# Kernel optimization log

Measured on AMD Instinct MI355X. Metric: run time of the kernel, lower is better.

## Reference

```python
import jax, jax.numpy as jnp
import numpy as np

B, NP1, D = 64, 1025, 256  # N+1 tokens, feature dim d (label dim makes d+1)
N_LAYER, N_HEAD = 4, 4
VAR = 0.02


def _pad_pq(allparam):
    """Build padded (d+1)x(d+1) P_full/Q_full for all layers/heads at once.
    P_full gets a 1 at [d, d]; Q_full is zero-padded."""
    L, H, _, d, _ = allparam.shape
    Pf = (jnp.zeros((L, H, d + 1, d + 1), allparam.dtype)
          .at[:, :, :d, :d].set(allparam[:, :, 0])
          .at[:, :, d, d].set(1.0))
    Qf = (jnp.zeros((L, H, d + 1, d + 1), allparam.dtype)
          .at[:, :, :d, :d].set(allparam[:, :, 1]))
    return Pf, Qf


def setup_inputs() -> dict:
    key = jax.random.key(0)
    k1, k2 = jax.random.split(key)
    Z = jax.random.normal(k1, (B, NP1, D + 1), dtype=jnp.float32)
    allparam = jax.random.normal(k2, (N_LAYER, N_HEAD, 2, D, D), dtype=jnp.float32) * VAR
    return {"Z": Z, "allparam": allparam}


def reference(Z, allparam):
    Bb, Np1, dp1 = Z.shape
    N = Np1 - 1
    Pf, Qf = _pad_pq(allparam)  # (L, H, d+1, d+1)
    # mask A = diag(1,...,1,0): equivalent to zeroing the last key token
    mask = jnp.ones((Np1,), Z.dtype).at[N].set(0.0)
    for l in range(allparam.shape[0]):
        # attn[b,h,n,m] = Z[b,n,:] @ Q_full[h] @ Z[b,m,:]
        attn = jnp.einsum('bni,hij,bmj->bhnm', Z, Qf[l], Z)
        attn = jax.nn.relu(attn)
        # key[b,h,m,i] = P_full[h] @ Z[b,m,:], last token masked out (A matrix)
        key_t = jnp.einsum('hij,bmj->bhmi', Pf[l], Z) * mask[None, None, :, None]
        # sum over heads fused into the einsum reduction; scale by 1/N
        res = jnp.einsum('bhnm,bhmi->bni', attn, key_t) / N
        Z = Z + res  # residual connection
    return Z
```

## Files before the change

kernel.cpp:

```cpp
#include <hip/hip_runtime.h>
#include <cstdint>
#include <cstddef>

#define B_    64
#define NP1   1025
#define N_    1024
#define D_    256
#define DP1   257
#define L_    4
#define H_    4
#define MT    1024
#define NCHE  32
#define IPAD  272
#define TR_   1024

typedef __bf16 bf16;
typedef bf16 bf16x4 __attribute__((ext_vector_type(4)));
typedef bf16 bf16x8 __attribute__((ext_vector_type(8)));
typedef float f32x4 __attribute__((ext_vector_type(4)));

__device__ __forceinline__ f32x4 mfma16(bf16x8 a, bf16x8 b, f32x4 c) {
    return __builtin_amdgcn_mfma_f32_16x16x32_bf16(a, b, c, 0, 0, 0);
}

__device__ __forceinline__ void async16(const void* g, void* l) {
    __builtin_amdgcn_global_load_lds(
        (const __attribute__((address_space(1))) void*)g,
        (__attribute__((address_space(3))) void*)l, 16, 0, 0);
}

__global__ void k_prep_pq(const float* __restrict__ ap,
                          bf16* __restrict__ Pb, bf16* __restrict__ Qt) {
    int idx = blockIdx.x * 256 + threadIdx.x;
    int j  = idx & 255;
    int i  = (idx >> 8) & 255;
    int lh = idx >> 16;
    const float* base = ap + (size_t)lh * 2 * D_ * D_;
    float p = base[i * D_ + j];
    float q = base[D_ * D_ + i * D_ + j];
    Pb[((size_t)lh * D_ + i) * D_ + j] = (bf16)p;
    Qt[((size_t)lh * D_ + j) * D_ + i] = (bf16)q;
}

__global__ __launch_bounds__(256) void k_zbt(const float* __restrict__ Z,
                                             bf16* __restrict__ Zb,
                                             bf16* __restrict__ ZbT) {
    __shared__ float t[64][65];
    int m0 = blockIdx.x * 64, j0 = blockIdx.y * 64, b = blockIdx.z;
    int c = threadIdx.x & 63, r0 = threadIdx.x >> 6;
#pragma unroll
    for (int s = 0; s < 16; s++) {
        int r = s * 4 + r0;
        int j = j0 + c;
        float v = (j < DP1) ? Z[((size_t)b * NP1 + m0 + r) * DP1 + j] : 0.f;
        t[r][c] = v;
        if (j < D_) Zb[((size_t)b * N_ + m0 + r) * D_ + j] = (bf16)v;
    }
    __syncthreads();
#pragma unroll
    for (int s = 0; s < 16; s++) {
        int rr = s * 4 + r0;
        int j = j0 + rr;
        if (j < DP1)
            ZbT[((size_t)b * DP1 + j) * MT + m0 + c] = (bf16)t[c][rr];
    }
}

__global__ __launch_bounds__(512, 1) void k_attn(const bf16* __restrict__ Zb,
                                                 const bf16* __restrict__ ZbT,
                                                 const bf16* __restrict__ Qt,
                                                 const bf16* __restrict__ Pb,
                                                 float* __restrict__ Z,
                                                 bf16* __restrict__ T,
                                                 bf16* __restrict__ Tlab,
                                                 int layer) {
    __shared__ bf16 zbS[2][32][256];
    __shared__ bf16 ztS[2][IPAD][32];
    __shared__ bf16 sl[8][32][40];

    const int tid  = threadIdx.x;
    const int id   = blockIdx.x;
    const int wave = tid >> 6, lane = tid & 63;
    const int quad = lane >> 4, l16 = lane & 15;

    const int xcd = id & 7, u = id >> 3;
    const int b   = xcd + 8 * (u & 7);
    const int bx  = u >> 3;
    const int n0w = bx * 256 + wave * 32;

    const bf16* Zbb  = Zb  + (size_t)b * N_ * D_;
    const bf16* ZbTb = ZbT + (size_t)b * DP1 * MT;

    const int zrow  = wave * 2 + (lane >> 5);
    const int zscol = ((lane & 31) ^ (zrow & 7)) * 8;
    const int krow  = wave * 16 + (lane >> 2);
    const int kscol = ((lane & 3) ^ ((lane >> 3) & 3)) * 8;
    const int xs    = l16 & 7;
    const int kf    = (l16 >> 1) & 3;

    auto stage = [&](int mc_, int p_) {
        int m0 = mc_ * 32;
        const bf16* zsrc = Zbb + (size_t)(m0 + zrow) * D_ + zscol;
#pragma unroll
        for (int t = 0; t < 2; t++)
            async16(zsrc + (size_t)t * 16 * D_, &zbS[p_][t * 16 + wave * 2][0]);
        const bf16* ksrc = ZbTb + (size_t)krow * MT + m0 + kscol;
#pragma unroll
        for (int t = 0; t < 2; t++)
            async16(ksrc + (size_t)t * 128 * MT, &ztS[p_][t * 128 + wave * 16][0]);
        if (wave == 0)
            async16(ksrc + (size_t)256 * MT, &ztS[p_][256][0]);
    };

    int p = 0;

    for (int h = 0; h < H_; h++) {
        const bf16* Qth = Qt + (size_t)(layer * H_ + h) * D_ * D_;

        if (h == 0) stage(0, 0);

        f32x4 acc[2][17];
#pragma unroll
        for (int ns = 0; ns < 2; ns++)
#pragma unroll
            for (int it = 0; it < 17; it++) acc[ns][it] = (f32x4){0.f, 0.f, 0.f, 0.f};

        bf16x8 zqa[2][8];
#pragma unroll 2
        for (int jc = 0; jc < 8; jc++) {
            f32x4 c00 = (f32x4){0.f,0.f,0.f,0.f}, c01 = c00, c10 = c00, c11 = c00;
#pragma unroll
            for (int kc = 0; kc < 8; kc++) {
                const bf16* qb = Qth + (size_t)(jc * 32 + l16) * D_ + kc * 32 + quad * 8;
                const bf16* az = Zbb + (size_t)(n0w + l16) * D_ + kc * 32 + quad * 8;
                bf16x8 q0 = *(const bf16x8*)(qb);
                bf16x8 q1 = *(const bf16x8*)(qb + 16 * D_);
                bf16x8 a0 = *(const bf16x8*)(az);
                bf16x8 a1 = *(const bf16x8*)(az + 16 * D_);
                c00 = mfma16(q0, a0, c00);
                c01 = mfma16(q0, a1, c01);
                c10 = mfma16(q1, a0, c10);
                c11 = mfma16(q1, a1, c11);
            }
            f32x4 cv[2][2] = {{c00, c01}, {c10, c11}};
#pragma unroll
            for (int jt = 0; jt < 2; jt++)
#pragma unroll
                for (int ns = 0; ns < 2; ns++) {
                    bf16x4 pk;
#pragma unroll
                    for (int r = 0; r < 4; r++) pk[r] = (bf16)cv[jt][ns][r];
                    *(bf16x4*)(&sl[wave][ns * 16 + l16][jt * 16 + quad * 4]) = pk;
                }
#pragma unroll
            for (int ns = 0; ns < 2; ns++)
                zqa[ns][jc] = *(const bf16x8*)(&sl[wave][ns * 16 + l16][quad * 8]);
        }

        if (h == 0) {
            asm volatile("s_waitcnt vmcnt(0)" ::: "memory");
            __builtin_amdgcn_s_barrier();
            __builtin_amdgcn_sched_barrier(0);
        }

        for (int cc = 0; cc < NCHE; cc++) {
            const bool haveNext = (cc + 1 < NCHE);
            if (haveNext) {
                int mcn = (h & 1) ? (NCHE - 2 - cc) : (cc + 1);
                stage(mcn, p ^ 1);
                if (wave == 0) asm volatile("s_waitcnt vmcnt(5)" ::: "memory");
                else           asm volatile("s_waitcnt vmcnt(4)" ::: "memory");
            } else {
                asm volatile("s_waitcnt vmcnt(0)" ::: "memory");
            }
            __builtin_amdgcn_s_barrier();
            __builtin_amdgcn_sched_barrier(0);

#pragma unroll
            for (int mt = 0; mt < 2; mt++) {
                f32x4 st0 = (f32x4){0.f,0.f,0.f,0.f}, st1 = st0;
                const bf16* zr = &zbS[p][mt * 16 + l16][0];
                __builtin_amdgcn_s_setprio(1);
#pragma unroll
                for (int kc = 0; kc < 8; kc++) {
                    bf16x8 az = *(const bf16x8*)(zr + (((kc * 4 + quad) ^ xs) * 8));
                    st0 = mfma16(az, zqa[0][kc], st0);
                    st1 = mfma16(az, zqa[1][kc], st1);
                }
                __builtin_amdgcn_s_setprio(0);
                bf16x4 p0, p1;
#pragma unroll
                for (int r = 0; r < 4; r++) {
                    p0[r] = (bf16)(st0[r] > 0.f ? st0[r] : 0.f);
                    p1[r] = (bf16)(st1[r] > 0.f ? st1[r] : 0.f);
                }
                *(bf16x4*)(&sl[wave][l16][mt * 16 + quad * 4])      = p0;
                *(bf16x4*)(&sl[wave][16 + l16][mt * 16 + quad * 4]) = p1;
            }
            bf16x8 sfrag[2];
#pragma unroll
            for (int ns = 0; ns < 2; ns++)
                sfrag[ns] = *(const bf16x8*)(&sl[wave][ns * 16 + l16][quad * 8]);

            __builtin_amdgcn_s_setprio(1);
#pragma unroll
            for (int it = 0; it < 17; it++) {
                const bf16* kr = &ztS[p][it * 16 + l16][0];
                bf16x8 bk = *(const bf16x8*)(kr + ((quad ^ kf) * 8));
                acc[0][it] = mfma16(sfrag[0], bk, acc[0][it]);
                acc[1][it] = mfma16(sfrag[1], bk, acc[1][it]);
            }
            __builtin_amdgcn_s_setprio(0);

            __builtin_amdgcn_sched_barrier(0);
            __builtin_amdgcn_s_barrier();
            if (haveNext) p ^= 1;
        }

        bf16* Th  = T    + (size_t)(b * H_ + h) * TR_ * D_;
        bf16* Tlh = Tlab + (size_t)(b * H_ + h) * TR_;
#pragma unroll
        for (int ns = 0; ns < 2; ns++)
#pragma unroll
            for (int it = 0; it < 17; it++)
#pragma unroll
                for (int r = 0; r < 4; r++) {
                    int n = n0w + ns * 16 + quad * 4 + r;
                    float v = acc[ns][it][r];
                    if (it < 16)
                        Th[(size_t)n * D_ + it * 16 + l16] = (bf16)v;
                    else if (l16 == 0)
                        Tlh[n] = (bf16)v;
                }
    }

    __syncthreads();
    {
        f32x4 acc2[2][16];
#pragma unroll
        for (int ns = 0; ns < 2; ns++)
#pragma unroll
            for (int it = 0; it < 16; it++) acc2[ns][it] = (f32x4){0.f, 0.f, 0.f, 0.f};

        for (int h = 0; h < H_; h++) {
            const bf16* Th = T  + (size_t)(b * H_ + h) * TR_ * D_;
            const bf16* Ph = Pb + (size_t)(layer * H_ + h) * D_ * D_;
#pragma unroll 2
            for (int kc = 0; kc < 8; kc++) {
                bf16x8 af[2];
#pragma unroll
                for (int ns = 0; ns < 2; ns++) {
                    int row = n0w + ns * 16 + l16;
                    af[ns] = *(const bf16x8*)(Th + (size_t)row * D_ + kc * 32 + quad * 8);
                }
#pragma unroll
                for (int it = 0; it < 16; it++) {
                    bf16x8 bp = *(const bf16x8*)(Ph + (size_t)(it * 16 + l16) * D_ + kc * 32 + quad * 8);
                    acc2[0][it] = mfma16(af[0], bp, acc2[0][it]);
                    acc2[1][it] = mfma16(af[1], bp, acc2[1][it]);
                }
            }
        }

        const float inv = 1.0f / (float)N_;
#pragma unroll
        for (int ns = 0; ns < 2; ns++)
#pragma unroll
            for (int it = 0; it < 16; it++) {
                const int i = it * 16 + l16;
                const int nbase = n0w + ns * 16 + quad * 4;
#pragma unroll
                for (int r = 0; r < 4; r++) {
                    size_t zi = ((size_t)b * NP1 + nbase + r) * DP1 + i;
                    Z[zi] += acc2[ns][it][r] * inv;
                }
            }
        if (tid < 256) {
            int n = bx * 256 + tid;
            float s = 0.f;
#pragma unroll
            for (int h = 0; h < H_; h++)
                s += (float)Tlab[(size_t)(b * H_ + h) * TR_ + n];
            Z[((size_t)b * NP1 + n) * DP1 + D_] += s * inv;
        }
    }

    if (bx == 0) {
        __syncthreads();
        float* lz1 = (float*)&zbS[0][0][0];
        float* lzq = lz1 + 256;
        float* lsS = lzq + 1024;
        float* lT  = lsS + 4096;
        if (tid < 256) lz1[tid] = Z[((size_t)b * NP1 + N_) * DP1 + tid];
        __syncthreads();
        {
            int j = tid & 255, hh = tid >> 8;
            for (int h2 = hh; h2 < H_; h2 += 2) {
                const bf16* qr = Qt + ((size_t)(layer * H_ + h2) * D_ + j) * D_;
                float a = 0.f;
                for (int i8 = 0; i8 < 32; i8++) {
                    bf16x8 q = *(const bf16x8*)(qr + i8 * 8);
#pragma unroll
                    for (int k = 0; k < 8; k++) a += lz1[i8 * 8 + k] * (float)q[k];
                }
                lzq[h2 * 256 + j] = a;
            }
        }
        __syncthreads();
        for (int m = tid; m < N_; m += 512) {
            const bf16* zr = Zbb + (size_t)m * D_;
            float a0 = 0.f, a1 = 0.f, a2 = 0.f, a3 = 0.f;
            for (int j8 = 0; j8 < 32; j8++) {
                bf16x8 z8 = *(const bf16x8*)(zr + j8 * 8);
#pragma unroll
                for (int k = 0; k < 8; k++) {
                    float zv = (float)z8[k];
                    int j = j8 * 8 + k;
                    a0 += lzq[j] * zv;
                    a1 += lzq[256 + j] * zv;
                    a2 += lzq[512 + j] * zv;
                    a3 += lzq[768 + j] * zv;
                }
            }
            lsS[m]        = a0 > 0.f ? a0 : 0.f;
            lsS[1024 + m] = a1 > 0.f ? a1 : 0.f;
            lsS[2048 + m] = a2 > 0.f ? a2 : 0.f;
            lsS[3072 + m] = a3 > 0.f ? a3 : 0.f;
        }
        __syncthreads();
        if (tid < DP1) {
            const bf16* tr2 = ZbTb + (size_t)tid * MT;
            float t0 = 0.f, t1 = 0.f, t2 = 0.f, t3 = 0.f;
            for (int m8 = 0; m8 < 128; m8++) {
                bf16x8 t8 = *(const bf16x8*)(tr2 + m8 * 8);
#pragma unroll
                for (int k = 0; k < 8; k++) {
                    float zv = (float)t8[k];
                    int m = m8 * 8 + k;
                    t0 += lsS[m] * zv;
                    t1 += lsS[1024 + m] * zv;
                    t2 += lsS[2048 + m] * zv;
                    t3 += lsS[3072 + m] * zv;
                }
            }
            lT[tid] = t0; lT[257 + tid] = t1; lT[514 + tid] = t2; lT[771 + tid] = t3;
        }
        __syncthreads();
        const float inv = 1.0f / (float)N_;
        if (tid < 256) {
            float out = 0.f;
            for (int h2 = 0; h2 < H_; h2++) {
                const bf16* pr = Pb + ((size_t)(layer * H_ + h2) * D_ + tid) * D_;
                for (int j8 = 0; j8 < 32; j8++) {
                    bf16x8 p8 = *(const bf16x8*)(pr + j8 * 8);
#pragma unroll
                    for (int k = 0; k < 8; k++)
                        out += lT[h2 * 257 + j8 * 8 + k] * (float)p8[k];
                }
            }
            Z[((size_t)b * NP1 + N_) * DP1 + tid] += out * inv;
        } else if (tid == 256) {
            float lab = lT[256] + lT[513] + lT[770] + lT[1027];
            Z[((size_t)b * NP1 + N_) * DP1 + D_] += lab * inv;
        }
    }
}

extern "C" void kernel_launch(void* const* d_in, const int* in_sizes, int n_in,
                              void* d_out, int out_size, void* d_ws, size_t ws_size,
                              hipStream_t stream) {
    const float* Zin = (const float*)d_in[0];
    const float* ap  = (const float*)d_in[1];
    float* Z = (float*)d_out;

    char* ws = (char*)d_ws;
    const size_t sz_Zb  = (size_t)B_ * N_ * D_ * sizeof(bf16);
    const size_t sz_ZbT = (size_t)B_ * DP1 * MT * sizeof(bf16);
    const size_t sz_T   = (size_t)B_ * H_ * TR_ * D_ * sizeof(bf16);
    const size_t sz_Tl  = (size_t)B_ * H_ * TR_ * sizeof(bf16);
    const size_t sz_P   = (size_t)L_ * H_ * D_ * D_ * sizeof(bf16);
    bf16* Zb  = (bf16*)ws;
    bf16* ZbT = (bf16*)(ws + sz_Zb);
    bf16* Tb  = (bf16*)(ws + sz_Zb + sz_ZbT);
    bf16* Tl  = (bf16*)(ws + sz_Zb + sz_ZbT + sz_T);
    bf16* Pb  = (bf16*)(ws + sz_Zb + sz_ZbT + sz_T + sz_Tl);
    bf16* Qt  = (bf16*)(ws + sz_Zb + sz_ZbT + sz_T + sz_Tl + sz_P);

    hipMemcpyAsync(Z, Zin, (size_t)B_ * NP1 * DP1 * sizeof(float),
                   hipMemcpyDeviceToDevice, stream);

    k_prep_pq<<<dim3((L_ * H_ * D_ * D_) / 256), 256, 0, stream>>>(ap, Pb, Qt);
    k_zbt<<<dim3(N_ / 64, 5, B_), 256, 0, stream>>>(Z, Zb, ZbT);

    for (int l = 0; l < L_; l++) {
        k_attn<<<dim3(256), 512, 0, stream>>>(Zb, ZbT, Qt, Pb, Z, Tb, Tl, l);
        if (l < L_ - 1)
            k_zbt<<<dim3(N_ / 64, 5, B_), 256, 0, stream>>>(Z, Zb, ZbT);
    }
}
```

Before: 3.199 ms.

## Split attention blocks into 256-thread halves with two blocks per CU

The attention kernel now launches 512 blocks of 256 threads, each covering 128 query rows instead of 256, with launch bounds of two blocks per CU. Async staging loops and vmcnt waits are adjusted for four waves. The per-wave LDS scratch is halved, so the two 16-row fragments are now written and read back in sequence. The intent is for lighter, independent blocks to overlap each other's barriers and staging. The cost is that every key/value chunk is staged twice per batch, so L2/global traffic doubles, and the serial last-row tail now runs on fewer threads.

```diff
diff --git a/kernel.cpp b/kernel.cpp
--- a/kernel.cpp
+++ b/kernel.cpp
@@ -66,7 +66,7 @@
     }
 }
 
-__global__ __launch_bounds__(512, 1) void k_attn(const bf16* __restrict__ Zb,
+__global__ __launch_bounds__(256, 2) void k_attn(const bf16* __restrict__ Zb,
                                                  const bf16* __restrict__ ZbT,
                                                  const bf16* __restrict__ Qt,
                                                  const bf16* __restrict__ Pb,
@@ -76,7 +76,7 @@
                                                  int layer) {
     __shared__ bf16 zbS[2][32][256];
     __shared__ bf16 ztS[2][IPAD][32];
-    __shared__ bf16 sl[8][32][40];
+    __shared__ bf16 sl[4][16][40];
 
     const int tid  = threadIdx.x;
     const int id   = blockIdx.x;
@@ -86,7 +86,7 @@
     const int xcd = id & 7, u = id >> 3;
     const int b   = xcd + 8 * (u & 7);
     const int bx  = u >> 3;
-    const int n0w = bx * 256 + wave * 32;
+    const int n0w = bx * 128 + wave * 32;
 
     const bf16* Zbb  = Zb  + (size_t)b * N_ * D_;
     const bf16* ZbTb = ZbT + (size_t)b * DP1 * MT;
@@ -102,12 +102,12 @@
         int m0 = mc_ * 32;
         const bf16* zsrc = Zbb + (size_t)(m0 + zrow) * D_ + zscol;
 #pragma unroll
-        for (int t = 0; t < 2; t++)
-            async16(zsrc + (size_t)t * 16 * D_, &zbS[p_][t * 16 + wave * 2][0]);
+        for (int t = 0; t < 4; t++)
+            async16(zsrc + (size_t)t * 8 * D_, &zbS[p_][t * 8 + wave * 2][0]);
         const bf16* ksrc = ZbTb + (size_t)krow * MT + m0 + kscol;
 #pragma unroll
-        for (int t = 0; t < 2; t++)
-            async16(ksrc + (size_t)t * 128 * MT, &ztS[p_][t * 128 + wave * 16][0]);
+        for (int t = 0; t < 4; t++)
+            async16(ksrc + (size_t)t * 64 * MT, &ztS[p_][t * 64 + wave * 16][0]);
         if (wave == 0)
             async16(ksrc + (size_t)256 * MT, &ztS[p_][256][0]);
     };
@@ -143,18 +143,23 @@
                 c11 = mfma16(q1, a1, c11);
             }
             f32x4 cv[2][2] = {{c00, c01}, {c10, c11}};
+            bf16x4 qsv[2];
+#pragma unroll
+            for (int jt = 0; jt < 2; jt++) {
+                bf16x4 pk0, pk1;
+#pragma unroll
+                for (int r = 0; r < 4; r++) {
+                    pk0[r] = (bf16)cv[jt][0][r];
+                    pk1[r] = (bf16)cv[jt][1][r];
+                }
+                *(bf16x4*)(&sl[wave][l16][jt * 16 + quad * 4]) = pk0;
+                qsv[jt] = pk1;
+            }
+            zqa[0][jc] = *(const bf16x8*)(&sl[wave][l16][quad * 8]);
 #pragma unroll
             for (int jt = 0; jt < 2; jt++)
-#pragma unroll
-                for (int ns = 0; ns < 2; ns++) {
-                    bf16x4 pk;
-#pragma unroll
-                    for (int r = 0; r < 4; r++) pk[r] = (bf16)cv[jt][ns][r];
-                    *(bf16x4*)(&sl[wave][ns * 16 + l16][jt * 16 + quad * 4]) = pk;
-                }
-#pragma unroll
-            for (int ns = 0; ns < 2; ns++)
-                zqa[ns][jc] = *(const bf16x8*)(&sl[wave][ns * 16 + l16][quad * 8]);
+                *(bf16x4*)(&sl[wave][l16][jt * 16 + quad * 4]) = qsv[jt];
+            zqa[1][jc] = *(const bf16x8*)(&sl[wave][l16][quad * 8]);
         }
 
         if (h == 0) {
@@ -168,14 +173,15 @@
             if (haveNext) {
                 int mcn = (h & 1) ? (NCHE - 2 - cc) : (cc + 1);
                 stage(mcn, p ^ 1);
-                if (wave == 0) asm volatile("s_waitcnt vmcnt(5)" ::: "memory");
-                else           asm volatile("s_waitcnt vmcnt(4)" ::: "memory");
+                if (wave == 0) asm volatile("s_waitcnt vmcnt(9)" ::: "memory");
+                else           asm volatile("s_waitcnt vmcnt(8)" ::: "memory");
             } else {
                 asm volatile("s_waitcnt vmcnt(0)" ::: "memory");
             }
             __builtin_amdgcn_s_barrier();
             __builtin_amdgcn_sched_barrier(0);
 
+            bf16x4 sv1[2];
 #pragma unroll
             for (int mt = 0; mt < 2; mt++) {
                 f32x4 st0 = (f32x4){0.f,0.f,0.f,0.f}, st1 = st0;
@@ -194,13 +200,15 @@
                     p0[r] = (bf16)(st0[r] > 0.f ? st0[r] : 0.f);
                     p1[r] = (bf16)(st1[r] > 0.f ? st1[r] : 0.f);
                 }
-                *(bf16x4*)(&sl[wave][l16][mt * 16 + quad * 4])      = p0;
-                *(bf16x4*)(&sl[wave][16 + l16][mt * 16 + quad * 4]) = p1;
+                *(bf16x4*)(&sl[wave][l16][mt * 16 + quad * 4]) = p0;
+                sv1[mt] = p1;
             }
             bf16x8 sfrag[2];
-#pragma unroll
-            for (int ns = 0; ns < 2; ns++)
-                sfrag[ns] = *(const bf16x8*)(&sl[wave][ns * 16 + l16][quad * 8]);
+            sfrag[0] = *(const bf16x8*)(&sl[wave][l16][quad * 8]);
+#pragma unroll
+            for (int mt = 0; mt < 2; mt++)
+                *(bf16x4*)(&sl[wave][l16][mt * 16 + quad * 4]) = sv1[mt];
+            sfrag[1] = *(const bf16x8*)(&sl[wave][l16][quad * 8]);
 
             __builtin_amdgcn_s_setprio(1);
 #pragma unroll
@@ -275,8 +283,8 @@
                     Z[zi] += acc2[ns][it][r] * inv;
                 }
             }
-        if (tid < 256) {
-            int n = bx * 256 + tid;
+        if (tid < 128) {
+            int n = bx * 128 + tid;
             float s = 0.f;
 #pragma unroll
             for (int h = 0; h < H_; h++)
@@ -291,23 +299,20 @@
         float* lzq = lz1 + 256;
         float* lsS = lzq + 1024;
         float* lT  = lsS + 4096;
-        if (tid < 256) lz1[tid] = Z[((size_t)b * NP1 + N_) * DP1 + tid];
+        lz1[tid] = Z[((size_t)b * NP1 + N_) * DP1 + tid];
         __syncthreads();
-        {
-            int j = tid & 255, hh = tid >> 8;
-            for (int h2 = hh; h2 < H_; h2 += 2) {
-                const bf16* qr = Qt + ((size_t)(layer * H_ + h2) * D_ + j) * D_;
-                float a = 0.f;
-                for (int i8 = 0; i8 < 32; i8++) {
-                    bf16x8 q = *(const bf16x8*)(qr + i8 * 8);
-#pragma unroll
-                    for (int k = 0; k < 8; k++) a += lz1[i8 * 8 + k] * (float)q[k];
-                }
-                lzq[h2 * 256 + j] = a;
-            }
+        for (int h2 = 0; h2 < H_; h2++) {
+            const bf16* qr = Qt + ((size_t)(layer * H_ + h2) * D_ + tid) * D_;
+            float a = 0.f;
+            for (int i8 = 0; i8 < 32; i8++) {
+                bf16x8 q = *(const bf16x8*)(qr + i8 * 8);
+#pragma unroll
+                for (int k = 0; k < 8; k++) a += lz1[i8 * 8 + k] * (float)q[k];
+            }
+            lzq[h2 * 256 + tid] = a;
         }
         __syncthreads();
-        for (int m = tid; m < N_; m += 512) {
+        for (int m = tid; m < N_; m += 256) {
             const bf16* zr = Zbb + (size_t)m * D_;
             float a0 = 0.f, a1 = 0.f, a2 = 0.f, a3 = 0.f;
             for (int j8 = 0; j8 < 32; j8++) {
@@ -328,8 +333,8 @@
             lsS[3072 + m] = a3 > 0.f ? a3 : 0.f;
         }
         __syncthreads();
-        if (tid < DP1) {
-            const bf16* tr2 = ZbTb + (size_t)tid * MT;
+        for (int j = tid; j < DP1; j += 256) {
+            const bf16* tr2 = ZbTb + (size_t)j * MT;
             float t0 = 0.f, t1 = 0.f, t2 = 0.f, t3 = 0.f;
             for (int m8 = 0; m8 < 128; m8++) {
                 bf16x8 t8 = *(const bf16x8*)(tr2 + m8 * 8);
@@ -343,11 +348,11 @@
                     t3 += lsS[3072 + m] * zv;
                 }
             }
-            lT[tid] = t0; lT[257 + tid] = t1; lT[514 + tid] = t2; lT[771 + tid] = t3;
+            lT[j] = t0; lT[257 + j] = t1; lT[514 + j] = t2; lT[771 + j] = t3;
         }
         __syncthreads();
         const float inv = 1.0f / (float)N_;
-        if (tid < 256) {
+        {
             float out = 0.f;
             for (int h2 = 0; h2 < H_; h2++) {
                 const bf16* pr = Pb + ((size_t)(layer * H_ + h2) * D_ + tid) * D_;
@@ -359,7 +364,8 @@
                 }
             }
             Z[((size_t)b * NP1 + N_) * DP1 + tid] += out * inv;
-        } else if (tid == 256) {
+        }
+        if (tid == 0) {
             float lab = lT[256] + lT[513] + lT[770] + lT[1027];
             Z[((size_t)b * NP1 + N_) * DP1 + D_] += lab * inv;
         }
@@ -393,7 +399,7 @@
     k_zbt<<<dim3(N_ / 64, 5, B_), 256, 0, stream>>>(Z, Zb, ZbT);
 
     for (int l = 0; l < L_; l++) {
-        k_attn<<<dim3(256), 512, 0, stream>>>(Zb, ZbT, Qt, Pb, Z, Tb, Tl, l);
+        k_attn<<<dim3(512), 256, 0, stream>>>(Zb, ZbT, Qt, Pb, Z, Tb, Tl, l);
         if (l < L_ - 1)
             k_zbt<<<dim3(N_ / 64, 5, B_), 256, 0, stream>>>(Z, Zb, ZbT);
     }
```

Result: no change. 3.226 ms (+0.9%).
